# Kernel tuning notes

Hardware: AMD Instinct MI355X
Metric: run time of the kernel (lower is better)

Reference implementation:

```python
import jax, jax.numpy as jnp
import numpy as np

N_FEAT = 256
NUM_HEADS = 8
EPS = 1e-12  # torch F.normalize default eps


def setup_inputs() -> dict:
    key = jax.random.key(0)
    k1, k2, k3 = jax.random.split(key, 3)
    b, c, h, w = 1, N_FEAT, 64, 64
    x = jax.random.normal(k1, (b, c, h, w), dtype=jnp.float32)
    # 1x1 convs == channel GEMMs; store as (out_ch, in_ch) matrices
    w_qkv = jax.random.normal(k2, (3 * c, c), dtype=jnp.float32) * (1.0 / np.sqrt(c))
    w_proj = jax.random.normal(k3, (c, c), dtype=jnp.float32) * (1.0 / np.sqrt(c))
    temperature = jnp.ones((NUM_HEADS, 1, 1), dtype=jnp.float32)
    return {"x": x, "w_qkv": w_qkv, "w_proj": w_proj, "temperature": temperature}


def _l2norm(t):
    n = jnp.linalg.norm(t, axis=-1, keepdims=True)
    return t / jnp.maximum(n, EPS)


def reference(x, w_qkv, w_proj, temperature):
    b, c, h, w = x.shape
    heads = temperature.shape[0]
    d = c // heads
    hw = h * w
    xf = x.reshape(b, c, hw)
    # qkv 1x1 conv: (b, 3c, hw)
    qkv = jnp.einsum('oc,bcs->bos', w_qkv, xf)
    qkv = qkv.reshape(b, 3, heads, d, hw)
    q, k, v = qkv[:, 0], qkv[:, 1], qkv[:, 2]  # (b, heads, d, hw)
    q = jnp.swapaxes(q, -2, -1)  # (b, heads, hw, d)
    k = jnp.swapaxes(k, -2, -1)
    v = jnp.swapaxes(v, -2, -1)
    q = _l2norm(q)
    k = _l2norm(k)
    attn = jnp.einsum('bhsd,bhtd->bhst', q, k) * temperature[None]  # (b, heads, hw, hw)
    attn = jax.nn.softmax(attn, axis=-1)
    out = jnp.einsum('bhst,bhtd->bhsd', attn, v)  # (b, heads, hw, d)
    # faithful to torch: permute(0,2,1,3).reshape(b,c,h,w)
    out = out.transpose(0, 2, 1, 3).reshape(b, c, h, w)
    out = jnp.einsum('oc,bchw->bohw', w_proj, out)
    return out
```

## Files before the change

kernel.cpp:

```cpp
#include <hip/hip_runtime.h>
#include <stdint.h>

#define HW 4096
#define NH 8
#define NSPLIT 4
#define TSPLIT (HW / NSPLIT)

typedef __attribute__((ext_vector_type(8))) short short8;
typedef __attribute__((ext_vector_type(4))) short s4b;
typedef __attribute__((ext_vector_type(4))) float floatx4;

__device__ inline float bf2f(uint16_t u) {
  union { uint32_t i; float f; } v; v.i = ((uint32_t)u) << 16; return v.f;
}
__device__ inline float bflo(uint32_t u) {
  union { uint32_t i; float f; } v; v.i = u << 16; return v.f;
}
__device__ inline float bfhi(uint32_t u) {
  union { uint32_t i; float f; } v; v.i = u & 0xFFFF0000u; return v.f;
}
__device__ inline uint16_t f2bf(float f) {
  union { float f; uint32_t i; } v; v.f = f;
  uint32_t u = v.i; u += 0x7fffu + ((u >> 16) & 1u); return (uint16_t)(u >> 16);
}
__device__ inline uint32_t pk2(float a, float b) {
  return (uint32_t)f2bf(a) | ((uint32_t)f2bf(b) << 16);
}
__device__ inline uint32_t asu(float f) { union { float f; uint32_t i; } v; v.f = f; return v.i; }
__device__ inline uint32_t pk2r(float a, float b) {
#if __has_builtin(__builtin_amdgcn_cvt_pk_bf16_f32)
  union { short2 s; uint32_t u; } x;
  x.s = __builtin_amdgcn_cvt_pk_bf16_f32(a, b);
  return x.u;
#else
  return __builtin_amdgcn_perm(asu(b) + 0x8000u, asu(a) + 0x8000u, 0x07060302u);
#endif
}
__device__ inline s4b mk_s4(uint32_t lo, uint32_t hi) {
  union { uint32_t u[2]; s4b s; } x; x.u[0] = lo; x.u[1] = hi; return x.s;
}
__device__ inline floatx4 mfma16(s4b a, s4b b, floatx4 c) {
#if __has_builtin(__builtin_amdgcn_mfma_f32_16x16x16bf16_1k)
  return __builtin_amdgcn_mfma_f32_16x16x16bf16_1k(a, b, c, 0, 0, 0);
#else
  floatx4 d = c;
  asm volatile("v_mfma_f32_16x16x16_bf16 %0, %1, %2, %0" : "+v"(d) : "v"(a), "v"(b));
  return d;
#endif
}
__device__ inline bool is_f32(const uint32_t* Tp32) { return (Tp32[0] & 0xFFFFu) == 0u; }
__device__ inline float read_temp(const void* Tp, int h) {
  if (is_f32((const uint32_t*)Tp)) return ((const float*)Tp)[h];
  return bf2f(((const uint16_t*)Tp)[h]);
}

__global__ __launch_bounds__(256) void k_gemm_qkv(const void* __restrict__ X,
                                                  const void* __restrict__ A,
                                                  const void* __restrict__ Tp,
                                                  uint16_t* __restrict__ Qr,
                                                  uint16_t* __restrict__ Kr,
                                                  uint16_t* __restrict__ Vr) {
  __shared__ uint16_t sA[128 * 64];
  __shared__ uint16_t sB[64 * 64];
  __shared__ uint16_t sXr[64 * 66];
  int tid = threadIdx.x;
  int w = tid >> 6, lane = tid & 63, lm = lane & 15, qd = lane >> 4;
  int n0 = blockIdx.x * 64, m0 = blockIdx.y * 128;
  bool aF32 = is_f32((const uint32_t*)Tp);
  floatx4 acc[2][4];
#pragma unroll
  for (int i = 0; i < 2; ++i)
#pragma unroll
    for (int j = 0; j < 4; ++j) acc[i][j] = (floatx4){0.f, 0.f, 0.f, 0.f};

  for (int k0 = 0; k0 < 256; k0 += 64) {
    __syncthreads();
    {
      int cl = tid >> 2, sc = (tid & 3) * 16;
      uint32_t* l32 = (uint32_t*)sXr;
      int base = (cl * 66 + sc) >> 1;
      if (aF32) {
        const float4* x4 = (const float4*)((const float*)X + (k0 + cl) * HW + n0 + sc);
        float4 a = x4[0], b = x4[1], c = x4[2], d = x4[3];
        l32[base + 0] = pk2(a.x, a.y); l32[base + 1] = pk2(a.z, a.w);
        l32[base + 2] = pk2(b.x, b.y); l32[base + 3] = pk2(b.z, b.w);
        l32[base + 4] = pk2(c.x, c.y); l32[base + 5] = pk2(c.z, c.w);
        l32[base + 6] = pk2(d.x, d.y); l32[base + 7] = pk2(d.z, d.w);
      } else {
        const uint4* xp = (const uint4*)((const uint16_t*)X + (k0 + cl) * HW + n0 + sc);
        uint4 a = xp[0], b = xp[1];
        l32[base + 0] = a.x; l32[base + 1] = a.y; l32[base + 2] = a.z; l32[base + 3] = a.w;
        l32[base + 4] = b.x; l32[base + 5] = b.y; l32[base + 6] = b.z; l32[base + 7] = b.w;
      }
    }
#pragma unroll
    for (int r = 0; r < 4; ++r) {
      int ch = r * 256 + tid; int row = ch >> 3, c8 = ch & 7;
      uint4 v;
      if (aF32) {
        const float4* s4 = (const float4*)((const float*)A + (m0 + row) * 256 + k0 + c8 * 8);
        float4 a = s4[0], b = s4[1];
        v = make_uint4(pk2(a.x, a.y), pk2(a.z, a.w), pk2(b.x, b.y), pk2(b.z, b.w));
      } else {
        v = *(const uint4*)((const uint16_t*)A + (m0 + row) * 256 + k0 + c8 * 8);
      }
      *(uint4*)(&sA[row * 64 + (c8 ^ (row & 7)) * 8]) = v;
    }
    __syncthreads();
    {
      int sl = tid >> 2, cs = (tid & 3) * 16;
      uint32_t wb[8];
#pragma unroll
      for (int j = 0; j < 8; ++j) {
        uint32_t lo = sXr[(cs + 2 * j) * 66 + sl];
        uint32_t hi = sXr[(cs + 2 * j + 1) * 66 + sl];
        wb[j] = lo | (hi << 16);
      }
      int c8 = cs >> 3;
      *(uint4*)(&sB[sl * 64 + ((c8 ^ (sl & 7))) * 8]) =
          make_uint4(wb[0], wb[1], wb[2], wb[3]);
      *(uint4*)(&sB[sl * 64 + (((c8 + 1) ^ (sl & 7))) * 8]) =
          make_uint4(wb[4], wb[5], wb[6], wb[7]);
    }
    __syncthreads();
#pragma unroll
    for (int kk = 0; kk < 2; ++kk) {
      short8 af[2];
#pragma unroll
      for (int mt = 0; mt < 2; ++mt) {
        int row = w * 32 + mt * 16 + lm;
        af[mt] = *(const short8*)(&sA[row * 64 + ((kk * 4 + qd) ^ (row & 7)) * 8]);
      }
#pragma unroll
      for (int nt = 0; nt < 4; ++nt) {
        int row = nt * 16 + lm;
        short8 bf = *(const short8*)(&sB[row * 64 + ((kk * 4 + qd) ^ (row & 7)) * 8]);
#pragma unroll
        for (int mt = 0; mt < 2; ++mt)
          acc[mt][nt] = __builtin_amdgcn_mfma_f32_16x16x32_bf16(af[mt], bf, acc[mt][nt], 0, 0, 0);
      }
    }
  }
  int ow = m0 + w * 32;
  int type = ow >> 8;
  int hh = (ow >> 5) & 7;
  float tv = read_temp(Tp, hh);
#pragma unroll
  for (int nt = 0; nt < 4; ++nt) {
    int s = n0 + nt * 16 + lm;
    if (type < 2) {
      float ssq = 0.f;
#pragma unroll
      for (int mt = 0; mt < 2; ++mt)
#pragma unroll
        for (int r = 0; r < 4; ++r) ssq += acc[mt][nt][r] * acc[mt][nt][r];
      ssq += __shfl_xor(ssq, 16, 64);
      ssq += __shfl_xor(ssq, 32, 64);
      float sc = (type == 0 ? tv : 1.0f) / fmaxf(sqrtf(ssq), 1e-12f);
      uint16_t* dst = (type == 0 ? Qr : Kr) + ((hh << 12) + s) * 32;
#pragma unroll
      for (int mt = 0; mt < 2; ++mt)
        *(uint2*)(dst + mt * 16 + qd * 4) =
            make_uint2(pk2r(acc[mt][nt][0] * sc, acc[mt][nt][1] * sc),
                       pk2r(acc[mt][nt][2] * sc, acc[mt][nt][3] * sc));
    } else {
#pragma unroll
      for (int mt = 0; mt < 2; ++mt)
#pragma unroll
        for (int r = 0; r < 4; ++r)
          Vr[(hh * 32 + mt * 16 + qd * 4 + r) * HW + s] = f2bf(acc[mt][nt][r]);
    }
  }
}

__global__ __launch_bounds__(256, 4) void k_attn(const uint16_t* __restrict__ Qr,
                                                 const uint16_t* __restrict__ Kr,
                                                 const uint16_t* __restrict__ Vr,
                                                 const void* __restrict__ Tp,
                                                 uint16_t* __restrict__ Op,
                                                 float* __restrict__ Lp) {
  __shared__ uint16_t sK[256 * 32];
  __shared__ uint16_t sV[32 * 256];
  int tid = threadIdx.x;
  int w = tid >> 6, lane = tid & 63, lm = lane & 15, qd = lane >> 4;
  int bid = blockIdx.x;
  int h = bid & 7;
  int j = bid >> 3;
  int sp = j & 3;
  int qb = j >> 2;
  int srow = qb * 128 + w * 32;
  const float c1 = 1.44269504088896340736f;
  float c2 = fabsf(read_temp(Tp, h)) * c1;
  short8 qf0 = *(const short8*)(Qr + ((h << 12) + srow + lm) * 32 + qd * 8);
  short8 qf1 = *(const short8*)(Qr + ((h << 12) + srow + 16 + lm) * 32 + qd * 8);
  const uint16_t* Kg = Kr + (h << 12) * 32;
  const uint16_t* Vg = Vr + (h * 32) * HW;
  floatx4 o00 = {0.f, 0.f, 0.f, 0.f}, o01 = {0.f, 0.f, 0.f, 0.f};
  floatx4 o10 = {0.f, 0.f, 0.f, 0.f}, o11 = {0.f, 0.f, 0.f, 0.f};
  floatx4 l0 = {0.f, 0.f, 0.f, 0.f}, l1 = {0.f, 0.f, 0.f, 0.f};
  const s4b ones = mk_s4(0x3F803F80u, 0x3F803F80u);

  int rK = tid >> 2, cK = tid & 3;
  uint16_t* dk0 = &sK[rK * 32 + (cK ^ ((rK >> 1) & 3)) * 8];
  const uint16_t* gk0 = Kg + (sp * TSPLIT + rK) * 32 + cK * 8;
  int dVb = tid >> 5, cVx = tid & 31;
  int s0x = dVb >> 1;
  bool sw = dVb & 1;
  uint16_t* dv0 = &sV[dVb * 256 + (cVx ^ s0x) * 8];
  uint16_t* dv1 = &sV[(dVb + 8) * 256 + (cVx ^ s0x ^ 4) * 8];
  const uint16_t* gv0 = Vg + dVb * HW + sp * TSPLIT + cVx * 8;

  uint4 rk0 = *(const uint4*)gk0;
  uint4 rk1 = *(const uint4*)(gk0 + 2048);
  uint4 rk2 = *(const uint4*)(gk0 + 4096);
  uint4 rk3 = *(const uint4*)(gk0 + 6144);
  uint4 rv0 = *(const uint4*)gv0;
  uint4 rv1 = *(const uint4*)(gv0 + 8 * HW);
  uint4 rv2 = *(const uint4*)(gv0 + 16 * HW);
  uint4 rv3 = *(const uint4*)(gv0 + 24 * HW);

  for (int i = 0; i < TSPLIT / 256; ++i) {
    __syncthreads();
    *(uint4*)dk0 = rk0;
    *(uint4*)(dk0 + 2048) = rk1;
    *(uint4*)(dk0 + 4096) = rk2;
    *(uint4*)(dk0 + 6144) = rk3;
    *(uint4*)dv0 = sw ? make_uint4(rv0.z, rv0.w, rv0.x, rv0.y) : rv0;
    *(uint4*)(dv0 + 4096) = sw ? make_uint4(rv2.z, rv2.w, rv2.x, rv2.y) : rv2;
    *(uint4*)dv1 = sw ? make_uint4(rv1.z, rv1.w, rv1.x, rv1.y) : rv1;
    *(uint4*)(dv1 + 4096) = sw ? make_uint4(rv3.z, rv3.w, rv3.x, rv3.y) : rv3;
    if (i + 1 < TSPLIT / 256) {
      gk0 += 256 * 32; gv0 += 256;
      rk0 = *(const uint4*)gk0;
      rk1 = *(const uint4*)(gk0 + 2048);
      rk2 = *(const uint4*)(gk0 + 4096);
      rk3 = *(const uint4*)(gk0 + 6144);
      rv0 = *(const uint4*)gv0;
      rv1 = *(const uint4*)(gv0 + 8 * HW);
      rv2 = *(const uint4*)(gv0 + 16 * HW);
      rv3 = *(const uint4*)(gv0 + 24 * HW);
    }
    asm volatile("s_waitcnt lgkmcnt(0)\n\ts_barrier" ::: "memory");
#pragma unroll
    for (int nt = 0; nt < 16; ++nt) {
      int krow = nt * 16 + lm;
      short8 kf = *(const short8*)(&sK[krow * 32 + (qd ^ ((lm >> 1) & 3)) * 8]);
      int gp = (nt * 4 + qd) ^ lm;
      s4b v0 = *(const s4b*)(&sV[lm * 256 + gp * 4]);
      s4b v1 = *(const s4b*)(&sV[(lm + 16) * 256 + gp * 4]);
      floatx4 z = {0.f, 0.f, 0.f, 0.f};
      floatx4 sv = __builtin_amdgcn_mfma_f32_16x16x32_bf16(kf, qf0, z, 0, 0, 0);
      float p0 = __builtin_amdgcn_exp2f(fmaf(sv[0], c1, -c2));
      float p1 = __builtin_amdgcn_exp2f(fmaf(sv[1], c1, -c2));
      float p2 = __builtin_amdgcn_exp2f(fmaf(sv[2], c1, -c2));
      float p3 = __builtin_amdgcn_exp2f(fmaf(sv[3], c1, -c2));
      s4b pa = mk_s4(pk2r(p0, p1), pk2r(p2, p3));
      o00 = mfma16(pa, v0, o00);
      o01 = mfma16(pa, v1, o01);
      l0 = mfma16(pa, ones, l0);
      sv = __builtin_amdgcn_mfma_f32_16x16x32_bf16(kf, qf1, z, 0, 0, 0);
      p0 = __builtin_amdgcn_exp2f(fmaf(sv[0], c1, -c2));
      p1 = __builtin_amdgcn_exp2f(fmaf(sv[1], c1, -c2));
      p2 = __builtin_amdgcn_exp2f(fmaf(sv[2], c1, -c2));
      p3 = __builtin_amdgcn_exp2f(fmaf(sv[3], c1, -c2));
      pa = mk_s4(pk2r(p0, p1), pk2r(p2, p3));
      o10 = mfma16(pa, v0, o10);
      o11 = mfma16(pa, v1, o11);
      l1 = mfma16(pa, ones, l1);
    }
  }
  int sb = (sp * NH + h) * HW + srow;
  uint16_t* op = Op + (size_t)sb * 32;
#pragma unroll
  for (int r = 0; r < 4; ++r) {
    op[(qd * 4 + r) * 32 + lm] = f2bf(o00[r]);
    op[(qd * 4 + r) * 32 + 16 + lm] = f2bf(o01[r]);
    op[(16 + qd * 4 + r) * 32 + lm] = f2bf(o10[r]);
    op[(16 + qd * 4 + r) * 32 + 16 + lm] = f2bf(o11[r]);
  }
  if (lm == 0) {
#pragma unroll
    for (int r = 0; r < 4; ++r) {
      Lp[sb + qd * 4 + r] = l0[r];
      Lp[sb + 16 + qd * 4 + r] = l1[r];
    }
  }
}

__global__ __launch_bounds__(256) void k_comb(const uint16_t* __restrict__ Op,
                                              const float* __restrict__ Lp,
                                              uint16_t* __restrict__ Yt) {
  int gid = blockIdx.x * 256 + threadIdx.x;
  int g = gid >> 1, d0 = (gid & 1) * 16;
  int h = g >> 12, s = g & 4095;
  float L = 0.f;
  float a[16];
#pragma unroll
  for (int j = 0; j < 16; ++j) a[j] = 0.f;
#pragma unroll
  for (int sp = 0; sp < NSPLIT; ++sp) {
    int gj = sp * NH * HW + g;
    L += Lp[gj];
    const uint4* p = (const uint4*)(Op + (size_t)gj * 32 + d0);
    uint4 x = p[0], y = p[1];
    a[0] += bflo(x.x); a[1] += bfhi(x.x); a[2] += bflo(x.y); a[3] += bfhi(x.y);
    a[4] += bflo(x.z); a[5] += bfhi(x.z); a[6] += bflo(x.w); a[7] += bfhi(x.w);
    a[8] += bflo(y.x); a[9] += bfhi(y.x); a[10] += bflo(y.y); a[11] += bfhi(y.y);
    a[12] += bflo(y.z); a[13] += bfhi(y.z); a[14] += bflo(y.w); a[15] += bfhi(y.w);
  }
  float inv = __builtin_amdgcn_rcpf(L);
  int pbase = ((s & 15) << 8) + h * 32 + d0;
  int cp = s >> 4;
#pragma unroll
  for (int j = 0; j < 16; ++j) Yt[(pbase + j) * 256 + cp] = f2bf(a[j] * inv);
}

__global__ __launch_bounds__(256) void k_gemm_proj(const void* __restrict__ A,
                                                   const uint16_t* __restrict__ Bt,
                                                   void* __restrict__ C,
                                                   const uint32_t* __restrict__ Tp32) {
  __shared__ uint16_t sA[64 * 64];
  __shared__ uint16_t sB[32 * 64];
  int tid = threadIdx.x;
  int w = tid >> 6, lane = tid & 63, lm = lane & 15, qd = lane >> 4;
  int n0 = blockIdx.x * 32, m0 = blockIdx.y * 64;
  bool aF32 = is_f32(Tp32);
  floatx4 acc[2];
  acc[0] = (floatx4){0.f, 0.f, 0.f, 0.f};
  acc[1] = (floatx4){0.f, 0.f, 0.f, 0.f};

  for (int k0 = 0; k0 < 256; k0 += 64) {
    __syncthreads();
#pragma unroll
    for (int r = 0; r < 2; ++r) {
      int ch = r * 256 + tid; int row = ch >> 3, c8 = ch & 7;
      uint4 v;
      if (aF32) {
        const float4* s4 = (const float4*)((const float*)A + (m0 + row) * 256 + k0 + c8 * 8);
        float4 a = s4[0], b = s4[1];
        v = make_uint4(pk2(a.x, a.y), pk2(a.z, a.w), pk2(b.x, b.y), pk2(b.z, b.w));
      } else {
        v = *(const uint4*)((const uint16_t*)A + (m0 + row) * 256 + k0 + c8 * 8);
      }
      *(uint4*)(&sA[row * 64 + (c8 ^ (row & 7)) * 8]) = v;
    }
    {
      int row = tid >> 3, c8 = tid & 7;
      uint4 v = *(const uint4*)(Bt + (n0 + row) * 256 + k0 + c8 * 8);
      *(uint4*)(&sB[row * 64 + (c8 ^ (row & 7)) * 8]) = v;
    }
    __syncthreads();
#pragma unroll
    for (int kk = 0; kk < 2; ++kk) {
      int arow = w * 16 + lm;
      short8 af = *(const short8*)(&sA[arow * 64 + ((kk * 4 + qd) ^ (arow & 7)) * 8]);
#pragma unroll
      for (int nt = 0; nt < 2; ++nt) {
        int row = nt * 16 + lm;
        short8 bf = *(const short8*)(&sB[row * 64 + ((kk * 4 + qd) ^ (row & 7)) * 8]);
        acc[nt] = __builtin_amdgcn_mfma_f32_16x16x32_bf16(af, bf, acc[nt], 0, 0, 0);
      }
    }
  }
  bool f32o = is_f32(Tp32);
#pragma unroll
  for (int nt = 0; nt < 2; ++nt)
#pragma unroll
    for (int r = 0; r < 4; ++r) {
      int row = m0 + w * 16 + qd * 4 + r;
      int col = n0 + nt * 16 + lm;
      if (f32o) ((float*)C)[row * HW + col] = acc[nt][r];
      else ((uint16_t*)C)[row * HW + col] = f2bf(acc[nt][r]);
    }
}

extern "C" void kernel_launch(void* const* d_in, const int* in_sizes, int n_in,
                              void* d_out, int out_size, void* d_ws, size_t ws_size,
                              hipStream_t stream) {
  const void* X  = d_in[0];
  const void* Wq = d_in[1];
  const void* Wp = d_in[2];
  const void* Tp = d_in[3];
  const uint32_t* Tp32 = (const uint32_t*)Tp;
  uint16_t* ws = (uint16_t*)d_ws;
  uint16_t* Qr = ws;
  uint16_t* Kr = Qr + NH * HW * 32;
  uint16_t* Vr = Kr + NH * HW * 32;
  uint16_t* Yt = Vr + NH * 32 * HW;
  uint16_t* Op = Yt + 4096 * 256;
  float* Lp = (float*)(Op + (size_t)NSPLIT * NH * HW * 32);

  k_gemm_qkv<<<dim3(64, 6), 256, 0, stream>>>(X, Wq, Tp, Qr, Kr, Vr);
  k_attn<<<dim3(1024), 256, 0, stream>>>(Qr, Kr, Vr, Tp, Op, Lp);
  k_comb<<<dim3(256), 256, 0, stream>>>(Op, Lp, Yt);
  k_gemm_proj<<<dim3(128, 4), 256, 0, stream>>>(Wp, Yt, d_out, Tp32);
}
```

Baseline: 120.1 us.

## Fuse split-K attention combine into projection GEMM B-tile load

Removes the separate combine kernel. The projection GEMM now reads the partial attention outputs and row sums directly, normalizes them, and transposes them through shared memory to build its B tile. This saves one launch and the write and reread of the intermediate Yt buffer. In exchange, each of the 4 M-blocks recomputes the same combine, adding redundant global reads, one extra barrier per k-step, and more shared memory. It also relies on a pk2r helper that must already exist in the file.

```diff
diff --git a/kernel.cpp b/kernel.cpp
--- a/kernel.cpp
+++ b/kernel.cpp
@@ -287,47 +287,24 @@
   }
 }
 
-__global__ __launch_bounds__(256) void k_comb(const uint16_t* __restrict__ Op,
-                                              const float* __restrict__ Lp,
-                                              uint16_t* __restrict__ Yt) {
-  int gid = blockIdx.x * 256 + threadIdx.x;
-  int g = gid >> 1, d0 = (gid & 1) * 16;
-  int h = g >> 12, s = g & 4095;
-  float L = 0.f;
-  float a[16];
-#pragma unroll
-  for (int j = 0; j < 16; ++j) a[j] = 0.f;
-#pragma unroll
-  for (int sp = 0; sp < NSPLIT; ++sp) {
-    int gj = sp * NH * HW + g;
-    L += Lp[gj];
-    const uint4* p = (const uint4*)(Op + (size_t)gj * 32 + d0);
-    uint4 x = p[0], y = p[1];
-    a[0] += bflo(x.x); a[1] += bfhi(x.x); a[2] += bflo(x.y); a[3] += bfhi(x.y);
-    a[4] += bflo(x.z); a[5] += bfhi(x.z); a[6] += bflo(x.w); a[7] += bfhi(x.w);
-    a[8] += bflo(y.x); a[9] += bfhi(y.x); a[10] += bflo(y.y); a[11] += bfhi(y.y);
-    a[12] += bflo(y.z); a[13] += bfhi(y.z); a[14] += bflo(y.w); a[15] += bfhi(y.w);
-  }
-  float inv = __builtin_amdgcn_rcpf(L);
-  int pbase = ((s & 15) << 8) + h * 32 + d0;
-  int cp = s >> 4;
-#pragma unroll
-  for (int j = 0; j < 16; ++j) Yt[(pbase + j) * 256 + cp] = f2bf(a[j] * inv);
-}
-
 __global__ __launch_bounds__(256) void k_gemm_proj(const void* __restrict__ A,
-                                                   const uint16_t* __restrict__ Bt,
+                                                   const uint16_t* __restrict__ Op,
+                                                   const float* __restrict__ Lp,
                                                    void* __restrict__ C,
                                                    const uint32_t* __restrict__ Tp32) {
   __shared__ uint16_t sA[64 * 64];
   __shared__ uint16_t sB[32 * 64];
+  __shared__ float sOp[64 * 33];
   int tid = threadIdx.x;
   int w = tid >> 6, lane = tid & 63, lm = lane & 15, qd = lane >> 4;
   int n0 = blockIdx.x * 32, m0 = blockIdx.y * 64;
+  int h = (n0 >> 5) & 7, slo = n0 >> 8;
   bool aF32 = is_f32(Tp32);
   floatx4 acc[2];
   acc[0] = (floatx4){0.f, 0.f, 0.f, 0.f};
   acc[1] = (floatx4){0.f, 0.f, 0.f, 0.f};
+  int cl = tid >> 2, dp = (tid & 3) * 8;
+  int dd = tid >> 3, spart = (tid & 7) * 8;
 
   for (int k0 = 0; k0 < 256; k0 += 64) {
     __syncthreads();
@@ -345,9 +322,31 @@
       *(uint4*)(&sA[row * 64 + (c8 ^ (row & 7)) * 8]) = v;
     }
     {
-      int row = tid >> 3, c8 = tid & 7;
-      uint4 v = *(const uint4*)(Bt + (n0 + row) * 256 + k0 + c8 * 8);
-      *(uint4*)(&sB[row * 64 + (c8 ^ (row & 7)) * 8]) = v;
+      int s = slo + 16 * (k0 + cl);
+      float L = 0.f;
+      float a[8];
+#pragma unroll
+      for (int q = 0; q < 8; ++q) a[q] = 0.f;
+#pragma unroll
+      for (int sp = 0; sp < NSPLIT; ++sp) {
+        size_t gj = (size_t)(sp * NH + h) * HW + s;
+        L += Lp[gj];
+        uint4 x = *(const uint4*)(Op + gj * 32 + dp);
+        a[0] += bflo(x.x); a[1] += bfhi(x.x); a[2] += bflo(x.y); a[3] += bfhi(x.y);
+        a[4] += bflo(x.z); a[5] += bfhi(x.z); a[6] += bflo(x.w); a[7] += bfhi(x.w);
+      }
+      float inv = __builtin_amdgcn_rcpf(L);
+#pragma unroll
+      for (int q = 0; q < 8; ++q) sOp[cl * 33 + dp + q] = a[q] * inv;
+    }
+    __syncthreads();
+    {
+      float b[8];
+#pragma unroll
+      for (int q = 0; q < 8; ++q) b[q] = sOp[(spart + q) * 33 + dd];
+      *(uint4*)(&sB[dd * 64 + ((spart >> 3) ^ (dd & 7)) * 8]) =
+          make_uint4(pk2r(b[0], b[1]), pk2r(b[2], b[3]),
+                     pk2r(b[4], b[5]), pk2r(b[6], b[7]));
     }
     __syncthreads();
 #pragma unroll
@@ -386,12 +385,10 @@
   uint16_t* Qr = ws;
   uint16_t* Kr = Qr + NH * HW * 32;
   uint16_t* Vr = Kr + NH * HW * 32;
-  uint16_t* Yt = Vr + NH * 32 * HW;
-  uint16_t* Op = Yt + 4096 * 256;
+  uint16_t* Op = Vr + NH * 32 * HW;
   float* Lp = (float*)(Op + (size_t)NSPLIT * NH * HW * 32);
 
   k_gemm_qkv<<<dim3(64, 6), 256, 0, stream>>>(X, Wq, Tp, Qr, Kr, Vr);
   k_attn<<<dim3(1024), 256, 0, stream>>>(Qr, Kr, Vr, Tp, Op, Lp);
-  k_comb<<<dim3(256), 256, 0, stream>>>(Op, Lp, Yt);
-  k_gemm_proj<<<dim3(128, 4), 256, 0, stream>>>(Wp, Yt, d_out, Tp32);
-}
+  k_gemm_proj<<<dim3(128, 4), 256, 0, stream>>>(Wp, Op, Lp, d_out, Tp32);
+}
```

Measured after the change: 118.9 us. No clear change (-1.0%).
